# Kernel tuning notes

Measured on AMD Instinct MI355X. Metric: run time of the kernel, lower is better.

Reference implementation:

```python
import jax, jax.numpy as jnp
import numpy as np

EMB = 1024
HEADS = 16
HEAD_DIM = EMB // HEADS
EPS = 1e-5


def layer_norm(x, scale, shift):
    mean = jnp.mean(x, axis=-1, keepdims=True)
    var = jnp.mean(jnp.square(x - mean), axis=-1, keepdims=True)  # unbiased=False
    return scale * ((x - mean) / jnp.sqrt(var + EPS)) + shift


def gelu_tanh(x):
    c = jnp.sqrt(jnp.asarray(2.0 / jnp.pi, x.dtype))
    return 0.5 * x * (1.0 + jnp.tanh(c * (x + 0.044715 * x * x * x)))


def setup_inputs() -> dict:
    key = jax.random.key(0)
    ks = jax.random.split(key, 12)
    s = 0.02
    B, S, D = 2, 2048, EMB
    return {
        "x": jax.random.normal(ks[0], (B, S, D), jnp.float32),
        "wq": jax.random.normal(ks[1], (D, D), jnp.float32) * s,
        "wk": jax.random.normal(ks[2], (D, D), jnp.float32) * s,
        "wv": jax.random.normal(ks[3], (D, D), jnp.float32) * s,
        "wo": jax.random.normal(ks[4], (D, D), jnp.float32) * s,
        "bo": jnp.zeros((D,), jnp.float32),
        "w1": jax.random.normal(ks[5], (D, 4 * D), jnp.float32) * s,
        "b1": jnp.zeros((4 * D,), jnp.float32),
        "w2": jax.random.normal(ks[6], (4 * D, D), jnp.float32) * s,
        "b2": jnp.zeros((D,), jnp.float32),
        "g1": jnp.ones((D,), jnp.float32),
        "s1": jnp.zeros((D,), jnp.float32),
        "g2": jnp.ones((D,), jnp.float32),
        "s2": jnp.zeros((D,), jnp.float32),
    }


def reference(x, wq, wk, wv, wo, bo, w1, b1, w2, b2, g1, s1, g2, s2):
    B, S, D = x.shape
    # --- attention sub-block ---
    h = layer_norm(x, g1, s1)
    q = (h @ wq).reshape(B, S, HEADS, HEAD_DIM).transpose(0, 2, 1, 3)  # [B,H,S,d]
    k = (h @ wk).reshape(B, S, HEADS, HEAD_DIM).transpose(0, 2, 1, 3)
    v = (h @ wv).reshape(B, S, HEADS, HEAD_DIM).transpose(0, 2, 1, 3)
    scores = jnp.einsum("bhqd,bhkd->bhqk", q, k)
    causal = jnp.tril(jnp.ones((S, S), bool))  # True = keep
    scores = jnp.where(causal, scores, -jnp.inf)
    attn = jax.nn.softmax(scores / jnp.sqrt(jnp.asarray(HEAD_DIM, x.dtype)), axis=-1)
    ctx = jnp.einsum("bhqk,bhkd->bhqd", attn, v).transpose(0, 2, 1, 3).reshape(B, S, D)
    x = x + (ctx @ wo + bo)
    # --- FFN sub-block ---
    h = layer_norm(x, g2, s2)
    h = gelu_tanh(h @ w1 + b1) @ w2 + b2
    return x + h
```

## Files before the change

### kernel.cpp

```cpp
#include <hip/hip_runtime.h>


typedef __attribute__((ext_vector_type(8))) short s16x8;
typedef __attribute__((ext_vector_type(4))) float f32x4;
typedef __attribute__((ext_vector_type(16))) float f32x16;
typedef unsigned short u16;
typedef unsigned int u32;

#define DEV static __device__ __forceinline__
#define MFMA16 __builtin_amdgcn_mfma_f32_16x16x32_bf16
#define MFMA32 __builtin_amdgcn_mfma_f32_32x32x16_bf16
#define GLOAD_LDS16(gp, lp)                                         \
  __builtin_amdgcn_global_load_lds(                                 \
      (const __attribute__((address_space(1))) void*)(gp),          \
      (__attribute__((address_space(3))) void*)(lp), 16, 0, 0)

DEV u16 f2bf(float f) {
  union { float f; unsigned u; } c; c.f = f;
  unsigned u = c.u;
  u += 0x7fff + ((u >> 16) & 1);
  return (u16)(u >> 16);
}

DEV u32 cvtpk(float lo, float hi) {
  u32 r;
  asm("v_cvt_pk_bf16_f32 %0, %1, %2" : "=v"(r) : "v"(lo), "v"(hi));
  return r;
}

DEV float gelu_tanh(float v) {
  const float c0 = 0.7978845608028654f;
  float u = c0 * (v + 0.044715f * v * v * v);
  return 0.5f * v * (1.0f + tanhf(u));
}

DEV s16x8 ld8(const u16* p) { return *(const s16x8*)p; }

__global__ __launch_bounds__(256) void tconv_kernel(
    const float* __restrict__ W, u16* __restrict__ Wt, int K, int N) {
  __shared__ u16 T[64][80];
  const int t = threadIdx.x;
  const int n0 = blockIdx.x * 64, k0 = blockIdx.y * 64;
  const int kr = t >> 4, nc = (t & 15) * 4;
#pragma unroll
  for (int p = 0; p < 4; ++p) {
    const int k = p * 16 + kr;
    float4 v = *(const float4*)(W + (size_t)(k0 + k) * N + n0 + nc);
    T[nc + 0][k] = f2bf(v.x);
    T[nc + 1][k] = f2bf(v.y);
    T[nc + 2][k] = f2bf(v.z);
    T[nc + 3][k] = f2bf(v.w);
  }
  __syncthreads();
  const int nr = t >> 2, kc = (t & 3) * 16;
  *(s16x8*)(Wt + (size_t)(n0 + nr) * K + k0 + kc) = *(const s16x8*)&T[nr][kc];
  *(s16x8*)(Wt + (size_t)(n0 + nr) * K + k0 + kc + 8) =
      *(const s16x8*)&T[nr][kc + 8];
}

__global__ __launch_bounds__(256) void ln_kernel(
    const float* __restrict__ x, const float* __restrict__ g,
    const float* __restrict__ b, u16* __restrict__ out) {
  const int row = blockIdx.x;
  const int t = threadIdx.x;
  const float* xr = x + (size_t)row * 1024;
  float4 v = *(const float4*)(xr + t * 4);
  float s = v.x + v.y + v.z + v.w;
  float ss = v.x * v.x + v.y * v.y + v.z * v.z + v.w * v.w;
#pragma unroll
  for (int off = 1; off < 64; off <<= 1) {
    s += __shfl_xor(s, off);
    ss += __shfl_xor(ss, off);
  }
  __shared__ float sb[4], ssb[4];
  const int w = t >> 6;
  if ((t & 63) == 0) { sb[w] = s; ssb[w] = ss; }
  __syncthreads();
  s = sb[0] + sb[1] + sb[2] + sb[3];
  ss = ssb[0] + ssb[1] + ssb[2] + ssb[3];
  const float mean = s * (1.0f / 1024.0f);
  const float var = ss * (1.0f / 1024.0f) - mean * mean;
  const float rstd = rsqrtf(var + 1e-5f);
  const int c = t * 4;
  ushort4 o;
  o.x = f2bf(g[c + 0] * ((v.x - mean) * rstd) + b[c + 0]);
  o.y = f2bf(g[c + 1] * ((v.y - mean) * rstd) + b[c + 1]);
  o.z = f2bf(g[c + 2] * ((v.z - mean) * rstd) + b[c + 2]);
  o.w = f2bf(g[c + 3] * ((v.w - mean) * rstd) + b[c + 3]);
  *(ushort4*)(out + (size_t)row * 1024 + c) = o;
}

DEV void gemm_stage(const u16* __restrict__ A, const u16* __restrict__ Bt,
                    int bm, int bn, int K, int kof, u16 (*Al)[32],
                    u16 (*Bl)[32], int w, int lane) {
  const int srow = lane >> 2;
  const int scol = ((lane & 3) ^ ((lane >> 3) & 3)) * 8;
#pragma unroll
  for (int p = 0; p < 2; ++p) {
    const int r0 = (w * 2 + p) * 16;
    GLOAD_LDS16(A + (size_t)(bm + r0 + srow) * K + kof + scol, &Al[r0][0]);
    GLOAD_LDS16(Bt + (size_t)(bn + r0 + srow) * K + kof + scol, &Bl[r0][0]);
  }
}

DEV void gemm_step(const u16 (*Al)[32], const u16 (*Bl)[32],
                   f32x4 (&acc)[4][4], int wm, int wn, int lr, int lg) {
  const int cs = (lg ^ ((lr >> 1) & 3)) * 8;
  s16x8 af[4], bf[4];
#pragma unroll
  for (int i = 0; i < 4; ++i) {
    af[i] = *(const s16x8*)&Al[wm + i * 16 + lr][cs];
    bf[i] = *(const s16x8*)&Bl[wn + i * 16 + lr][cs];
  }
#pragma unroll
  for (int i = 0; i < 4; ++i)
#pragma unroll
    for (int j = 0; j < 4; ++j)
      acc[i][j] = MFMA16(af[i], bf[j], acc[i][j], 0, 0, 0);
}

template <int EPI>
__global__ __launch_bounds__(256) void gemm_kernel(
    const u16* __restrict__ A, const u16* __restrict__ Bt,
    const float* __restrict__ bias, const float* __restrict__ res,
    void* __restrict__ Cv, int M, int N, int K) {
  __shared__ __align__(16) u16 Al[2][128][32];
  __shared__ __align__(16) u16 Bl[2][128][32];
  const int t = threadIdx.x;
  const int lane = t & 63, w = t >> 6;
  const int wm = (w >> 1) * 64, wn = (w & 1) * 64;
  int bid = blockIdx.y * gridDim.x + blockIdx.x;
  const int q8 = (gridDim.x * gridDim.y) >> 3;
  bid = (bid & 7) * q8 + (bid >> 3);
  const int bm = (bid / gridDim.x) * 128, bn = (bid % gridDim.x) * 128;
  const int lr = lane & 15, lg = lane >> 4;
  f32x4 acc[4][4] = {};
  const int nkt = K >> 5;

  gemm_stage(A, Bt, bm, bn, K, 0, Al[0], Bl[0], w, lane);
  __syncthreads();
  for (int kt = 0; kt < nkt - 1; ++kt) {
    const int cur = kt & 1;
    gemm_stage(A, Bt, bm, bn, K, (kt + 1) << 5, Al[cur ^ 1], Bl[cur ^ 1], w,
               lane);
    gemm_step(Al[cur], Bl[cur], acc, wm, wn, lr, lg);
    __syncthreads();
  }
  gemm_step(Al[(nkt - 1) & 1], Bl[(nkt - 1) & 1], acc, wm, wn, lr, lg);

#pragma unroll
  for (int i = 0; i < 4; ++i) {
    const int row = bm + wm + i * 16 + lg * 4;
#pragma unroll
    for (int j = 0; j < 4; ++j) {
      const int col = bn + wn + j * 16 + lr;
      if (EPI == 0) {
        const int bb = row >> 11, sloc = row & 2047;
        const int which = col >> 10, n = col & 1023;
        const int hh = n >> 6, dd = n & 63;
        u16* qbuf = (u16*)Cv;
        if (which == 2) {
          ushort4 o;
          o.x = f2bf(acc[i][j][0]); o.y = f2bf(acc[i][j][1]);
          o.z = f2bf(acc[i][j][2]); o.w = f2bf(acc[i][j][3]);
          *(ushort4*)(qbuf + 8388608 +
                      (size_t)((bb * 16 + hh) * 64 + dd) * 2048 + sloc) = o;
        } else {
          const float sc = (which == 0) ? 0.18033688011112042f : 1.0f;
          u16* dst = qbuf + (size_t)which * 4194304 +
                     ((size_t)(bb * 16 + hh) * 2048 + sloc) * 64 + dd;
#pragma unroll
          for (int e = 0; e < 4; ++e) dst[(size_t)e * 64] = f2bf(acc[i][j][e] * sc);
        }
      } else if (EPI == 1) {
        float* C = (float*)Cv;
        const float bs = bias[col];
#pragma unroll
        for (int e = 0; e < 4; ++e)
          C[(size_t)(row + e) * N + col] =
              acc[i][j][e] + bs + res[(size_t)(row + e) * N + col];
      } else {
        u16* C = (u16*)Cv;
        const float bs = bias[col];
#pragma unroll
        for (int e = 0; e < 4; ++e)
          C[(size_t)(row + e) * N + col] = f2bf(gelu_tanh(acc[i][j][e] + bs));
      }
    }
  }
}

DEV void g64_stage(const u16* __restrict__ A, const u16* __restrict__ Bt,
                   int bm, int bn, int K, int kof, u16 (*Al)[32],
                   u16 (*Bl)[32], int w, int lane) {
  const int srow = lane >> 2;
  const int scol = ((lane & 3) ^ ((lane >> 3) & 3)) * 8;
  const int r0 = w << 4;
  GLOAD_LDS16(A + (size_t)(bm + r0 + srow) * K + kof + scol, &Al[r0][0]);
  GLOAD_LDS16(Bt + (size_t)(bn + r0 + srow) * K + kof + scol, &Bl[r0][0]);
}

DEV void g64_step(const u16 (*Al)[32], const u16 (*Bl)[32],
                  f32x4 (&acc)[2][2], int wm, int wn, int lr, int lg) {
  const int cs = (lg ^ ((lr >> 1) & 3)) * 8;
  s16x8 af[2], bf[2];
#pragma unroll
  for (int i = 0; i < 2; ++i) {
    af[i] = *(const s16x8*)&Al[wm + i * 16 + lr][cs];
    bf[i] = *(const s16x8*)&Bl[wn + i * 16 + lr][cs];
  }
#pragma unroll
  for (int i = 0; i < 2; ++i)
#pragma unroll
    for (int j = 0; j < 2; ++j)
      acc[i][j] = MFMA16(af[i], bf[j], acc[i][j], 0, 0, 0);
}

template <int EPI>
__global__ __launch_bounds__(256) void gemm64_kernel(
    const u16* __restrict__ A, const u16* __restrict__ Bt,
    const float* __restrict__ bias, const float* __restrict__ res,
    void* __restrict__ Cv, int M, int N, int K) {
  __shared__ __align__(16) u16 Al[2][64][32];
  __shared__ __align__(16) u16 Bl[2][64][32];
  const int t = threadIdx.x;
  const int lane = t & 63, w = t >> 6;
  const int wm = (w >> 1) * 32, wn = (w & 1) * 32;
  int bid = blockIdx.y * gridDim.x + blockIdx.x;
  const int q8 = (gridDim.x * gridDim.y) >> 3;
  bid = (bid & 7) * q8 + (bid >> 3);
  const int bm = (bid / gridDim.x) * 64, bn = (bid % gridDim.x) * 64;
  const int lr = lane & 15, lg = lane >> 4;
  f32x4 acc[2][2] = {};
  const int nkt = K >> 5;

  g64_stage(A, Bt, bm, bn, K, 0, Al[0], Bl[0], w, lane);
  __syncthreads();
  for (int kt = 0; kt < nkt - 1; ++kt) {
    const int cur = kt & 1;
    g64_stage(A, Bt, bm, bn, K, (kt + 1) << 5, Al[cur ^ 1], Bl[cur ^ 1], w,
              lane);
    g64_step(Al[cur], Bl[cur], acc, wm, wn, lr, lg);
    __syncthreads();
  }
  g64_step(Al[(nkt - 1) & 1], Bl[(nkt - 1) & 1], acc, wm, wn, lr, lg);

#pragma unroll
  for (int i = 0; i < 2; ++i) {
    const int row = bm + wm + i * 16 + lg * 4;
#pragma unroll
    for (int j = 0; j < 2; ++j) {
      const int col = bn + wn + j * 16 + lr;
      if (EPI == 1) {
        float* C = (float*)Cv;
        const float bs = bias[col];
#pragma unroll
        for (int e = 0; e < 4; ++e)
          C[(size_t)(row + e) * N + col] =
              acc[i][j][e] + bs + res[(size_t)(row + e) * N + col];
      } else {
        u16* C = (u16*)Cv;
        const float bs = bias[col];
#pragma unroll
        for (int e = 0; e < 4; ++e)
          C[(size_t)(row + e) * N + col] = f2bf(gelu_tanh(acc[i][j][e] + bs));
      }
    }
  }
}

DEV void g256_stage(const u16* __restrict__ A, const u16* __restrict__ Bt,
                    int bm, int bn, int K, int kof, u16 (*Al)[32],
                    u16 (*Bl)[32], int w, int lane) {
  const int srow = lane >> 2;
  const int scol = ((lane & 3) ^ ((lane >> 3) & 3)) * 8;
#pragma unroll
  for (int c = 0; c < 2; ++c) {
    const int r0 = (w << 5) + (c << 4);
    GLOAD_LDS16(A + (size_t)(bm + r0 + srow) * K + kof + scol, &Al[r0][0]);
    GLOAD_LDS16(Bt + (size_t)(bn + r0 + srow) * K + kof + scol, &Bl[r0][0]);
  }
}

DEV void g256_step(const u16 (*Al)[32], const u16 (*Bl)[32],
                   f32x4 (&acc)[8][4], int wm, int wn, int lr, int lg) {
  const int cs = (lg ^ ((lr >> 1) & 3)) * 8;
  s16x8 af[8], bf[4];
#pragma unroll
  for (int i = 0; i < 8; ++i)
    af[i] = *(const s16x8*)&Al[wm + i * 16 + lr][cs];
#pragma unroll
  for (int j = 0; j < 4; ++j)
    bf[j] = *(const s16x8*)&Bl[wn + j * 16 + lr][cs];
#pragma unroll
  for (int i = 0; i < 8; ++i)
#pragma unroll
    for (int j = 0; j < 4; ++j)
      acc[i][j] = MFMA16(af[i], bf[j], acc[i][j], 0, 0, 0);
}

template <int EPI>
__global__ __launch_bounds__(512, 2) void gemm256_kernel(
    const u16* __restrict__ A, const u16* __restrict__ Bt,
    const float* __restrict__ bias, const float* __restrict__ res,
    void* __restrict__ Cv, int M, int N, int K) {
  __shared__ __align__(16) u16 Al[2][256][32];
  __shared__ __align__(16) u16 Bl[2][256][32];
  const int t = threadIdx.x;
  const int lane = t & 63, w = t >> 6;
  const int wm = (w >> 2) << 7;
  const int wn = (w & 3) << 6;
  int bid = blockIdx.y * gridDim.x + blockIdx.x;
  const int q8 = (gridDim.x * gridDim.y) >> 3;
  bid = (bid & 7) * q8 + (bid >> 3);
  const int bm = (bid / gridDim.x) << 8, bn = (bid % gridDim.x) << 8;
  const int lr = lane & 15, lg = lane >> 4;
  f32x4 acc[8][4] = {};
  const int nkt = K >> 5;

  g256_stage(A, Bt, bm, bn, K, 0, Al[0], Bl[0], w, lane);
  __syncthreads();
  for (int kt = 0; kt < nkt - 1; ++kt) {
    const int cur = kt & 1;
    g256_stage(A, Bt, bm, bn, K, (kt + 1) << 5, Al[cur ^ 1], Bl[cur ^ 1], w,
               lane);
    g256_step(Al[cur], Bl[cur], acc, wm, wn, lr, lg);
    __syncthreads();
  }
  g256_step(Al[(nkt - 1) & 1], Bl[(nkt - 1) & 1], acc, wm, wn, lr, lg);

#pragma unroll
  for (int i = 0; i < 8; ++i) {
    const int row = bm + wm + i * 16 + lg * 4;
#pragma unroll
    for (int j = 0; j < 4; ++j) {
      const int col = bn + wn + j * 16 + lr;
      if (EPI == 1) {
        float* C = (float*)Cv;
        const float bs = bias[col];
#pragma unroll
        for (int e = 0; e < 4; ++e)
          C[(size_t)(row + e) * N + col] =
              acc[i][j][e] + bs + res[(size_t)(row + e) * N + col];
      } else {
        u16* C = (u16*)Cv;
        const float bs = bias[col];
#pragma unroll
        for (int e = 0; e < 4; ++e)
          C[(size_t)(row + e) * N + col] = f2bf(gelu_tanh(acc[i][j][e] + bs));
      }
    }
  }
}

DEV float vmax16(const f32x16& v) {
  float a = fmaxf(v[0], v[1]), b = fmaxf(v[2], v[3]);
  float c = fmaxf(v[4], v[5]), d = fmaxf(v[6], v[7]);
  float e = fmaxf(v[8], v[9]), f = fmaxf(v[10], v[11]);
  float g = fmaxf(v[12], v[13]), h = fmaxf(v[14], v[15]);
  a = fmaxf(a, b); c = fmaxf(c, d); e = fmaxf(e, f); g = fmaxf(g, h);
  return fmaxf(fmaxf(a, c), fmaxf(e, g));
}
DEV float vsum16(const f32x16& v) {
  float a = v[0] + v[1], b = v[2] + v[3];
  float c = v[4] + v[5], d = v[6] + v[7];
  float e = v[8] + v[9], f = v[10] + v[11];
  float g = v[12] + v[13], h = v[14] + v[15];
  a += b; c += d; e += f; g += h;
  return (a + c) + (e + g);
}

struct A32 {
  s16x8 q[4];
  f32x16 o0, o1;
  float m, l;
};

template <int MODE>
DEV void body32(A32& st, int k0, const u16* Kb, const u16* Vb, int la,
                int hi) {
  s16x8 ka0[4], ka1[4];
#pragma unroll
  for (int c = 0; c < 4; ++c)
    ka0[c] = ld8(Kb + (size_t)(k0 + la) * 64 + c * 16 + hi * 8);
  if (MODE != 2)
#pragma unroll
    for (int c = 0; c < 4; ++c)
      ka1[c] = ld8(Kb + (size_t)(k0 + 32 + la) * 64 + c * 16 + hi * 8);
  f32x16 s0, s1;
#pragma unroll
  for (int r = 0; r < 16; ++r) { s0[r] = 0.f; s1[r] = 0.f; }
#pragma unroll
  for (int c = 0; c < 4; ++c) s0 = MFMA32(ka0[c], st.q[c], s0, 0, 0, 0);
  if (MODE != 2)
#pragma unroll
    for (int c = 0; c < 4; ++c) s1 = MFMA32(ka1[c], st.q[c], s1, 0, 0, 0);
  const int nkc = (MODE == 2) ? 2 : 4;
  s16x8 va0[4], va1[4];
#pragma unroll
  for (int kc = 0; kc < 4; ++kc)
    if (kc < nkc) {
      va0[kc] = ld8(Vb + (size_t)la * 2048 + k0 + kc * 16 + hi * 8);
      va1[kc] = ld8(Vb + (size_t)(32 + la) * 2048 + k0 + kc * 16 + hi * 8);
    }
  if (MODE == 1) {
#pragma unroll
    for (int r = 0; r < 16; ++r) {
      const int kl = (r & 3) + 8 * (r >> 2) + 4 * hi;
      if (kl > la) s1[r] = -INFINITY;
    }
  }
  if (MODE == 2) {
#pragma unroll
    for (int r = 0; r < 16; ++r) {
      const int kl = (r & 3) + 8 * (r >> 2) + 4 * hi;
      if (kl > la) s0[r] = -INFINITY;
    }
  }
  float mt = vmax16(s0);
  if (MODE != 2) mt = fmaxf(mt, vmax16(s1));
  mt = fmaxf(mt, __shfl_xor(mt, 32));
  const float mn = fmaxf(st.m, mt);
  const float sf = exp2f(st.m - mn);
#pragma unroll
  for (int r = 0; r < 16; ++r) s0[r] = exp2f(s0[r] - mn);
  if (MODE != 2)
#pragma unroll
    for (int r = 0; r < 16; ++r) s1[r] = exp2f(s1[r] - mn);
  float rs = vsum16(s0);
  if (MODE != 2) rs += vsum16(s1);
  rs += __shfl_xor(rs, 32);
  st.l = st.l * sf + rs;
  st.m = mn;
#pragma unroll
  for (int r = 0; r < 16; ++r) { st.o0[r] *= sf; st.o1[r] *= sf; }
  const int nh = (MODE == 2) ? 1 : 2;
#pragma unroll
  for (int half = 0; half < nh; ++half) {
    u32 w[8];
#pragma unroll
    for (int i = 0; i < 8; ++i)
      w[i] = half ? cvtpk(s1[2 * i], s1[2 * i + 1])
                  : cvtpk(s0[2 * i], s0[2 * i + 1]);
#pragma unroll
    for (int kp = 0; kp < 2; ++kp) {
      const u32 w0 = w[4 * kp + 0], w1 = w[4 * kp + 1];
      const u32 w2 = w[4 * kp + 2], w3 = w[4 * kp + 3];
      const u32 t0 = hi ? w0 : w2, t1 = hi ? w1 : w3;
      const u32 x0 = (u32)__shfl_xor((int)t0, 32);
      const u32 x1 = (u32)__shfl_xor((int)t1, 32);
      union { u32 u[4]; s16x8 v; } bb;
      bb.u[0] = hi ? x0 : w0;
      bb.u[1] = hi ? x1 : w1;
      bb.u[2] = hi ? w2 : x0;
      bb.u[3] = hi ? w3 : x1;
      const int kc = half * 2 + kp;
      st.o0 = MFMA32(va0[kc], bb.v, st.o0, 0, 0, 0);
      st.o1 = MFMA32(va1[kc], bb.v, st.o1, 0, 0, 0);
    }
  }
}

__global__ __launch_bounds__(64, 2) void attn_kernel(
    const u16* __restrict__ Qg, const u16* __restrict__ Kg,
    const u16* __restrict__ Vt, u16* __restrict__ ctx) {
  const int lane = threadIdx.x & 63;
  const int la = lane & 31, hi = lane >> 5;
  const int bh = blockIdx.x & 31;
  const int qc = 63 - (blockIdx.x >> 5);
  const int qs = qc * 32;
  const size_t baseK = (size_t)bh * 2048 * 64;
  const size_t baseV = (size_t)bh * 64 * 2048;
  const u16* Kb = Kg + baseK;
  const u16* Vb = Vt + baseV;

  A32 st;
#pragma unroll
  for (int c = 0; c < 4; ++c)
    st.q[c] = ld8(Qg + baseK + (size_t)(qs + la) * 64 + c * 16 + hi * 8);
#pragma unroll
  for (int r = 0; r < 16; ++r) { st.o0[r] = 0.f; st.o1[r] = 0.f; }
  st.m = -INFINITY;
  st.l = 0.f;

  const int nfull = qs >> 6;
  for (int kt = 0; kt < nfull; ++kt) body32<0>(st, kt * 64, Kb, Vb, la, hi);
  if (qs & 32) body32<1>(st, nfull * 64, Kb, Vb, la, hi);
  else         body32<2>(st, qs, Kb, Vb, la, hi);

  const int bb = bh >> 4, hh = bh & 15;
  const float inv = 1.0f / st.l;
  u16* crow = ctx + (size_t)(bb * 2048 + qs + la) * 1024 + hh * 64;
#pragma unroll
  for (int r = 0; r < 16; r += 2) {
    const int d = (r & 3) + 8 * (r >> 2) + 4 * hi;
    *(u32*)(crow + d) = cvtpk(st.o0[r] * inv, st.o0[r + 1] * inv);
    *(u32*)(crow + 32 + d) = cvtpk(st.o1[r] * inv, st.o1[r + 1] * inv);
  }
}

extern "C" void kernel_launch(void* const* d_in, const int* in_sizes, int n_in,
                              void* d_out, int out_size, void* d_ws,
                              size_t ws_size, hipStream_t stream) {
  const float* x  = (const float*)d_in[0];
  const float* wq = (const float*)d_in[1];
  const float* wk = (const float*)d_in[2];
  const float* wv = (const float*)d_in[3];
  const float* wo = (const float*)d_in[4];
  const float* bo = (const float*)d_in[5];
  const float* w1 = (const float*)d_in[6];
  const float* b1 = (const float*)d_in[7];
  const float* w2 = (const float*)d_in[8];
  const float* b2 = (const float*)d_in[9];
  const float* g1 = (const float*)d_in[10];
  const float* s1 = (const float*)d_in[11];
  const float* g2 = (const float*)d_in[12];
  const float* s2 = (const float*)d_in[13];
  float* out = (float*)d_out;

  const size_t MB = (size_t)1 << 20;
  char* p = (char*)d_ws;
  u16* hb    = (u16*)(p + 0 * MB);
  u16* qbuf  = (u16*)(p + 8 * MB);
  u16* ctxb  = (u16*)(p + 32 * MB);
  float* x2  = (float*)(p + 40 * MB);
  u16* h2b   = (u16*)(p + 56 * MB);
  u16* qkvw  = (u16*)(p + 64 * MB);
  u16* wot   = (u16*)(p + 70 * MB);
  u16* w1t   = (u16*)(p + 72 * MB);
  u16* w2t   = (u16*)(p + 80 * MB);
  u16* gb    = (u16*)(p + 0 * MB);

  const dim3 blk(256);
  tconv_kernel<<<dim3(16, 16), blk, 0, stream>>>(wq, qkvw, 1024, 1024);
  tconv_kernel<<<dim3(16, 16), blk, 0, stream>>>(wk, qkvw + 1048576, 1024, 1024);
  tconv_kernel<<<dim3(16, 16), blk, 0, stream>>>(wv, qkvw + 2097152, 1024, 1024);
  tconv_kernel<<<dim3(16, 16), blk, 0, stream>>>(wo, wot, 1024, 1024);
  tconv_kernel<<<dim3(64, 16), blk, 0, stream>>>(w1, w1t, 1024, 4096);
  tconv_kernel<<<dim3(16, 64), blk, 0, stream>>>(w2, w2t, 4096, 1024);

  ln_kernel<<<4096, blk, 0, stream>>>(x, g1, s1, hb);
  gemm_kernel<0><<<dim3(24, 32), blk, 0, stream>>>(hb, qkvw, nullptr, nullptr,
                                                   qbuf, 4096, 3072, 1024);
  attn_kernel<<<dim3(2048), dim3(64), 0, stream>>>(
      qbuf, qbuf + 4194304, qbuf + 8388608, ctxb);
  gemm64_kernel<1><<<dim3(16, 64), blk, 0, stream>>>(ctxb, wot, bo, x, x2,
                                                     4096, 1024, 1024);
  ln_kernel<<<4096, blk, 0, stream>>>(x2, g2, s2, h2b);
  gemm256_kernel<2><<<dim3(16, 16), dim3(512), 0, stream>>>(
      h2b, w1t, b1, nullptr, gb, 4096, 4096, 1024);
  gemm64_kernel<1><<<dim3(16, 64), blk, 0, stream>>>(gb, w2t, b2, x2, out,
                                                     4096, 1024, 4096);
}
```

Before: 307.3 us.

## Pair short and long causal query tiles per attention block for balance

Each attention workgroup now handles two 32-row query tiles, tA and 63-tA, so every block does about the same amount of causal work. The two tiles' online-softmax states are interleaved over the key tiles they share, so each K/V tile is reused across both. This halves the grid to 1024 blocks and removes the occupancy hint of 2 from the launch bounds. Holding two accumulator states per wave raises register pressure and may lower occupancy or cause spills.

```diff
diff --git a/kernel.cpp b/kernel.cpp
--- a/kernel.cpp
+++ b/kernel.cpp
@@ -461,42 +461,69 @@
   }
 }
 
-__global__ __launch_bounds__(64, 2) void attn_kernel(
+DEV void a32_init(A32& st, const u16* Qbase, int qs, int la, int hi) {
+#pragma unroll
+  for (int c = 0; c < 4; ++c)
+    st.q[c] = ld8(Qbase + (size_t)(qs + la) * 64 + c * 16 + hi * 8);
+#pragma unroll
+  for (int r = 0; r < 16; ++r) { st.o0[r] = 0.f; st.o1[r] = 0.f; }
+  st.m = -INFINITY;
+  st.l = 0.f;
+}
+
+DEV void a32_fin(const A32& st, u16* __restrict__ ctx, int bh, int qs, int la,
+                 int hi) {
+  const int bb = bh >> 4, hh = bh & 15;
+  const float inv = 1.0f / st.l;
+  u16* crow = ctx + (size_t)(bb * 2048 + qs + la) * 1024 + hh * 64;
+#pragma unroll
+  for (int r = 0; r < 16; r += 2) {
+    const int d = (r & 3) + 8 * (r >> 2) + 4 * hi;
+    *(u32*)(crow + d) = cvtpk(st.o0[r] * inv, st.o0[r + 1] * inv);
+    *(u32*)(crow + 32 + d) = cvtpk(st.o1[r] * inv, st.o1[r + 1] * inv);
+  }
+}
+
+template <bool ODD>
+DEV void chain_tail(A32& st, int nfull, int qs, const u16* Kb, const u16* Vb,
+                    int la, int hi) {
+  if (ODD) body32<1>(st, nfull * 64, Kb, Vb, la, hi);
+  else     body32<2>(st, qs, Kb, Vb, la, hi);
+}
+
+__global__ __launch_bounds__(64) void attn_kernel(
     const u16* __restrict__ Qg, const u16* __restrict__ Kg,
     const u16* __restrict__ Vt, u16* __restrict__ ctx) {
   const int lane = threadIdx.x & 63;
   const int la = lane & 31, hi = lane >> 5;
-  const int bh = blockIdx.x & 31;
-  const int qc = 63 - (blockIdx.x >> 5);
-  const int qs = qc * 32;
+  const int tA = blockIdx.x;
+  const int bh = blockIdx.y;
+  const int tB = 63 - tA;
+  const int qsA = tA * 32, qsB = tB * 32;
+  const int nfA = tA >> 1, nfB = tB >> 1;
   const size_t baseK = (size_t)bh * 2048 * 64;
   const size_t baseV = (size_t)bh * 64 * 2048;
   const u16* Kb = Kg + baseK;
   const u16* Vb = Vt + baseV;
 
-  A32 st;
-#pragma unroll
-  for (int c = 0; c < 4; ++c)
-    st.q[c] = ld8(Qg + baseK + (size_t)(qs + la) * 64 + c * 16 + hi * 8);
-#pragma unroll
-  for (int r = 0; r < 16; ++r) { st.o0[r] = 0.f; st.o1[r] = 0.f; }
-  st.m = -INFINITY;
-  st.l = 0.f;
-
-  const int nfull = qs >> 6;
-  for (int kt = 0; kt < nfull; ++kt) body32<0>(st, kt * 64, Kb, Vb, la, hi);
-  if (qs & 32) body32<1>(st, nfull * 64, Kb, Vb, la, hi);
-  else         body32<2>(st, qs, Kb, Vb, la, hi);
-
-  const int bb = bh >> 4, hh = bh & 15;
-  const float inv = 1.0f / st.l;
-  u16* crow = ctx + (size_t)(bb * 2048 + qs + la) * 1024 + hh * 64;
-#pragma unroll
-  for (int r = 0; r < 16; r += 2) {
-    const int d = (r & 3) + 8 * (r >> 2) + 4 * hi;
-    *(u32*)(crow + d) = cvtpk(st.o0[r] * inv, st.o0[r + 1] * inv);
-    *(u32*)(crow + 32 + d) = cvtpk(st.o1[r] * inv, st.o1[r + 1] * inv);
-  }
+  A32 A, B;
+  a32_init(A, Qg + baseK, qsA, la, hi);
+  a32_init(B, Qg + baseK, qsB, la, hi);
+
+  for (int kt = 0; kt < nfA; ++kt) {
+    body32<0>(B, kt * 64, Kb, Vb, la, hi);
+    body32<0>(A, kt * 64, Kb, Vb, la, hi);
+  }
+  body32<0>(B, nfA * 64, Kb, Vb, la, hi);
+  if (tA & 1) chain_tail<true>(A, nfA, qsA, Kb, Vb, la, hi);
+  else        chain_tail<false>(A, nfA, qsA, Kb, Vb, la, hi);
+  a32_fin(A, ctx, bh, qsA, la, hi);
+
+  for (int kt = nfA + 1; kt < nfB; ++kt)
+    body32<0>(B, kt * 64, Kb, Vb, la, hi);
+  if (tB & 1) chain_tail<true>(B, nfB, qsB, Kb, Vb, la, hi);
+  else        chain_tail<false>(B, nfB, qsB, Kb, Vb, la, hi);
+  a32_fin(B, ctx, bh, qsB, la, hi);
 }
 
 extern "C" void kernel_launch(void* const* d_in, const int* in_sizes, int n_in,
@@ -542,7 +569,7 @@
   ln_kernel<<<4096, blk, 0, stream>>>(x, g1, s1, hb);
   gemm_kernel<0><<<dim3(24, 32), blk, 0, stream>>>(hb, qkvw, nullptr, nullptr,
                                                    qbuf, 4096, 3072, 1024);
-  attn_kernel<<<dim3(2048), dim3(64), 0, stream>>>(
+  attn_kernel<<<dim3(32, 32), dim3(64), 0, stream>>>(
       qbuf, qbuf + 4194304, qbuf + 8388608, ctxb);
   gemm64_kernel<1><<<dim3(16, 64), blk, 0, stream>>>(ctxb, wot, bo, x, x2,
                                                      4096, 1024, 1024);
```

Result: no change. 302.5 us (-1.6%).
